# Optimization experiments

Measured on AMD Instinct MI355X. Metric: run time of the kernel, lower is better.

Reference implementation:

```python
import jax, jax.numpy as jnp
import numpy as np

EMBED_DIM = 1024
NUM_HEADS = 16
HEAD_DIM = EMBED_DIM // NUM_HEADS


def setup_inputs() -> dict:
    key = jax.random.key(0)
    ks = jax.random.split(key, 12)
    B, Nq, Nkv, D = 4, 1024, 1024, EMBED_DIM
    s = 1.0 / np.sqrt(D)
    return {
        "query": jax.random.normal(ks[0], (B, Nq, D), jnp.float32),
        "key_value": jax.random.normal(ks[1], (B, Nkv, D), jnp.float32),
        "Wq": jax.random.normal(ks[2], (D, D), jnp.float32) * s,
        "bq": jnp.zeros((D,), jnp.float32),
        "Wk": jax.random.normal(ks[3], (D, D), jnp.float32) * s,
        "bk": jnp.zeros((D,), jnp.float32),
        "Wv": jax.random.normal(ks[4], (D, D), jnp.float32) * s,
        "bv": jnp.zeros((D,), jnp.float32),
        "Wo": jax.random.normal(ks[5], (D, D), jnp.float32) * s,
        "bo": jnp.zeros((D,), jnp.float32),
        "gamma": jnp.ones((D,), jnp.float32),
        "beta": jnp.zeros((D,), jnp.float32),
    }


def reference(query, key_value, Wq, bq, Wk, bk, Wv, bv, Wo, bo, gamma, beta):
    B, Nq, D = query.shape
    Nkv = key_value.shape[1]
    H, Hd = NUM_HEADS, HEAD_DIM
    # projections -> [B, H, N, Hd]
    q = (query @ Wq + bq).reshape(B, Nq, H, Hd).transpose(0, 2, 1, 3)
    k = (key_value @ Wk + bk).reshape(B, Nkv, H, Hd).transpose(0, 2, 1, 3)
    v = (key_value @ Wv + bv).reshape(B, Nkv, H, Hd).transpose(0, 2, 1, 3)
    scores = jnp.einsum("bhqd,bhkd->bhqk", q, k) / jnp.sqrt(jnp.float32(Hd))
    attn = jax.nn.softmax(scores, axis=-1)  # dropout = identity at eval
    out = jnp.einsum("bhqk,bhkd->bhqd", attn, v)
    out = out.transpose(0, 2, 1, 3).reshape(B, Nq, D)
    out = out @ Wo + bo
    # residual + LayerNorm (eps = 1e-5, torch default)
    x = query + out
    mu = jnp.mean(x, axis=-1, keepdims=True)
    var = jnp.mean(jnp.square(x - mu), axis=-1, keepdims=True)
    return (x - mu) / jnp.sqrt(var + 1e-5) * gamma + beta
```

## Files before the change

### kernel.cpp

```cpp
#include <hip/hip_runtime.h>

typedef unsigned short u16;
typedef unsigned int u32;
typedef __attribute__((ext_vector_type(2))) unsigned int u32x2;
typedef __attribute__((ext_vector_type(4))) unsigned short u16x4;
typedef __attribute__((ext_vector_type(8))) short short8;
typedef __attribute__((ext_vector_type(4))) float f32x4;

#define MFMA16(a, b, c) __builtin_amdgcn_mfma_f32_16x16x32_bf16(a, b, c, 0, 0, 0)

__device__ __forceinline__ u16 f2bf(float f) {
  unsigned u = __builtin_bit_cast(unsigned, f);
  u += 0x7fffu + ((u >> 16) & 1u);
  return (u16)(u >> 16);
}

__device__ __forceinline__ float bf2f(u16 b) {
  return __builtin_bit_cast(float, ((u32)b) << 16);
}

__device__ __forceinline__ u32 cvtpk(float lo, float hi) {
  u32 r;
  asm("v_cvt_pk_bf16_f32 %0, %1, %2" : "=v"(r) : "v"(lo), "v"(hi));
  return r;
}

__device__ __forceinline__ float ex2(float x) {
  float r;
  asm("v_exp_f32 %0, %1" : "=v"(r) : "v"(x));
  return r;
}

__device__ __forceinline__ void gl_lds16(const void* g, void* l) {
  __builtin_amdgcn_global_load_lds((const __attribute__((address_space(1))) char*)g,
                                   (__attribute__((address_space(3))) char*)l, 16, 0, 0);
}

__global__ __launch_bounds__(256) void cvt2_k(const float* __restrict__ a,
                                              const float* __restrict__ b,
                                              u16* __restrict__ oa, u16* __restrict__ ob) {
  const int bid = blockIdx.x;
  const float* in = (bid < 4096) ? a : b;
  u16* out = (bid < 4096) ? oa : ob;
  int i = (bid & 4095) * 256 + threadIdx.x;
  float4 v = ((const float4*)in)[i];
  u16x4 o;
  o.x = f2bf(v.x); o.y = f2bf(v.y); o.z = f2bf(v.z); o.w = f2bf(v.w);
  ((u16x4*)out)[i] = o;
}

__global__ __launch_bounds__(256) void wt_k(const float* __restrict__ W0, const float* __restrict__ W1,
                                            const float* __restrict__ W2, const float* __restrict__ W3,
                                            u16* __restrict__ T0, u16* __restrict__ T1,
                                            u16* __restrict__ T2, u16* __restrict__ T3) {
  const float* W; u16* T;
  switch (blockIdx.z) {
    case 0: W = W0; T = T0; break;
    case 1: W = W1; T = T1; break;
    case 2: W = W2; T = T2; break;
    default: W = W3; T = T3; break;
  }
  __shared__ __align__(16) u16 t[64][72];
  const int k0 = blockIdx.y * 64, n0 = blockIdx.x * 64;
  const int tid = threadIdx.x;
  const int r = tid >> 4, c4 = (tid & 15) * 4;
#pragma unroll
  for (int i = 0; i < 4; i++) {
    float4 v = *(const float4*)(W + (k0 + r + i * 16) * 1024 + n0 + c4);
    u16x4 o;
    o.x = f2bf(v.x); o.y = f2bf(v.y); o.z = f2bf(v.z); o.w = f2bf(v.w);
    *(u16x4*)&t[r + i * 16][c4] = o;
  }
  __syncthreads();
#pragma unroll
  for (int i = 0; i < 4; i++) {
    int nr = r + i * 16;
    u16x4 o;
    o.x = t[c4 + 0][nr]; o.y = t[c4 + 1][nr]; o.z = t[c4 + 2][nr]; o.w = t[c4 + 3][nr];
    *(u16x4*)(T + (n0 + nr) * 1024 + k0 + c4) = o;
  }
}

__global__ __launch_bounds__(256, 3) void gemmqkv_k(
    const u16* __restrict__ qbf, const u16* __restrict__ kvbf,
    const u16* __restrict__ Wqt, const u16* __restrict__ Wkt, const u16* __restrict__ Wvt,
    const float* __restrict__ pbq, const float* __restrict__ pbk, const float* __restrict__ pbv,
    u16* __restrict__ Qh, u16* __restrict__ Kh, u16* __restrict__ Vth) {
  const int lin = blockIdx.x;
  const int swz = (lin & 7) * 96 + (lin >> 3);
  const int x = swz & 7, y = (swz >> 3) & 31, z = swz >> 8;

  const u16* A  = (z == 0) ? qbf : kvbf;
  const u16* Bt = (z == 0) ? Wqt : (z == 1 ? Wkt : Wvt);
  const float* bias = (z == 0) ? pbq : (z == 1 ? pbk : pbv);

  __shared__ __align__(16) u16 As[128 * 64];
  __shared__ __align__(16) u16 Bs[128 * 64];
  const int tid = threadIdx.x;
  const int l = tid & 63, w = tid >> 6;
  const int lr = l >> 4, lc = l & 15;
  const int wr = w >> 1, wc = w & 1;
  const int m0 = y * 128, n0 = x * 128;

  f32x4 acc[4][4] = {};

  const int sr = tid >> 2, sc = (tid & 3) * 8;
  const u16* Ag = A + (m0 + sr) * 1024 + sc;
  const u16* Bg = Bt + (n0 + sr) * 1024 + sc;

  for (int k0 = 0; k0 < 1024; k0 += 64) {
    __syncthreads();
    gl_lds16(Ag + k0, As + tid * 8);
    gl_lds16(Ag + 64 * 1024 + k0, As + 2048 + tid * 8);
    gl_lds16(Bg + k0, Bs + tid * 8);
    gl_lds16(Bg + 64 * 1024 + k0, Bs + 2048 + tid * 8);
    gl_lds16(Ag + k0 + 32, As + 4096 + tid * 8);
    gl_lds16(Ag + 64 * 1024 + k0 + 32, As + 6144 + tid * 8);
    gl_lds16(Bg + k0 + 32, Bs + 4096 + tid * 8);
    gl_lds16(Bg + 64 * 1024 + k0 + 32, Bs + 6144 + tid * 8);
    __syncthreads();
    const u16* PA = (z == 2) ? Bs : As;
    const u16* PB = (z == 2) ? As : Bs;
    short8 af[4][2], bf[4][2];
    const int ks8 = lr * 8;
#pragma unroll
    for (int m = 0; m < 4; m++)
#pragma unroll
      for (int h = 0; h < 2; h++)
        af[m][h] = *(const short8*)(PA + h * 4096 + (wr * 64 + m * 16 + lc) * 32 + ks8);
#pragma unroll
    for (int n = 0; n < 4; n++)
#pragma unroll
      for (int h = 0; h < 2; h++)
        bf[n][h] = *(const short8*)(PB + h * 4096 + (wc * 64 + n * 16 + lc) * 32 + ks8);
#pragma unroll
    for (int m = 0; m < 4; m++)
#pragma unroll
      for (int n = 0; n < 4; n++) {
        acc[m][n] = MFMA16(af[m][0], bf[n][0], acc[m][n]);
        acc[m][n] = MFMA16(af[m][1], bf[n][1], acc[m][n]);
      }
  }

  if (z == 2) {
#pragma unroll
    for (int m = 0; m < 4; m++) {
#pragma unroll
      for (int r = 0; r < 4; r++) {
        int ncol = n0 + wr * 64 + m * 16 + lr * 4 + r;
        float bb = bias[ncol];
        int h = ncol >> 6, d = ncol & 63;
#pragma unroll
        for (int n = 0; n < 4; n++) {
          int tok = m0 + wc * 64 + n * 16 + lc;
          Vth[(((tok >> 10) * 16 + h) * 64 + d) * 1024 + (tok & 1023)] =
              f2bf(acc[m][n][r] + bb);
        }
      }
    }
  } else {
    u16* outb = (z == 0) ? Qh : Kh;
    const float scale = (z == 0) ? 0.18033688f : 1.0f;
#pragma unroll
    for (int m = 0; m < 4; m++)
#pragma unroll
      for (int n = 0; n < 4; n++) {
        int ncol = n0 + wc * 64 + n * 16 + lc;
        float bb = bias[ncol];
        int h = ncol >> 6, d = ncol & 63;
#pragma unroll
        for (int r = 0; r < 4; r++) {
          int tok = m0 + wr * 64 + m * 16 + lr * 4 + r;
          outb[(((tok >> 10) * 16 + h) * 1024 + (tok & 1023)) * 64 + d] =
              f2bf((acc[m][n][r] + bb) * scale);
        }
      }
  }
}

__global__ __launch_bounds__(256, 4) void gemmo_k(const u16* __restrict__ A,
                                                  const u16* __restrict__ Bt,
                                                  const float* __restrict__ bias,
                                                  u16* __restrict__ outb) {
  const int lin = blockIdx.x;
  const int swz = (lin & 7) * 64 + (lin >> 3);
  const int x = swz & 15, y = swz >> 4;

  __shared__ __align__(16) u16 As[128 * 64];
  __shared__ __align__(16) u16 Bs[64 * 64];
  const int tid = threadIdx.x;
  const int l = tid & 63, w = tid >> 6;
  const int lr = l >> 4, lc = l & 15;
  const int wr = w >> 1, wc = w & 1;
  const int m0 = y * 128, n0 = x * 64;

  f32x4 acc[4][2] = {};
  const int sc = (tid & 3) * 8;
  const u16* Ag = A + (m0 + (tid >> 2)) * 1024 + sc;
  const u16* Bg = Bt + (n0 + (tid >> 2)) * 1024 + sc;

  for (int k0 = 0; k0 < 1024; k0 += 64) {
    __syncthreads();
    gl_lds16(Ag + k0, As + tid * 8);
    gl_lds16(Ag + 64 * 1024 + k0, As + 2048 + tid * 8);
    gl_lds16(Bg + k0, Bs + tid * 8);
    gl_lds16(Ag + k0 + 32, As + 4096 + tid * 8);
    gl_lds16(Ag + 64 * 1024 + k0 + 32, As + 6144 + tid * 8);
    gl_lds16(Bg + k0 + 32, Bs + 2048 + tid * 8);
    __syncthreads();
    short8 af[4][2], bf[2][2];
    const int ks8 = lr * 8;
#pragma unroll
    for (int m = 0; m < 4; m++)
#pragma unroll
      for (int h = 0; h < 2; h++)
        af[m][h] = *(const short8*)(As + h * 4096 + (wr * 64 + m * 16 + lc) * 32 + ks8);
#pragma unroll
    for (int n = 0; n < 2; n++)
#pragma unroll
      for (int h = 0; h < 2; h++)
        bf[n][h] = *(const short8*)(Bs + h * 2048 + (wc * 32 + n * 16 + lc) * 32 + ks8);
#pragma unroll
    for (int m = 0; m < 4; m++)
#pragma unroll
      for (int n = 0; n < 2; n++) {
        acc[m][n] = MFMA16(af[m][0], bf[n][0], acc[m][n]);
        acc[m][n] = MFMA16(af[m][1], bf[n][1], acc[m][n]);
      }
  }
#pragma unroll
  for (int m = 0; m < 4; m++)
#pragma unroll
    for (int n = 0; n < 2; n++) {
      int ncol = n0 + wc * 32 + n * 16 + lc;
      float bb = bias[ncol];
#pragma unroll
      for (int r = 0; r < 4; r++) {
        int tok = m0 + wr * 64 + m * 16 + lr * 4 + r;
        outb[tok * 1024 + ncol] = f2bf(acc[m][n][r] + bb);
      }
    }
}

__global__ __launch_bounds__(256, 2) void attn_k(const u16* __restrict__ Q,
                                                 const u16* __restrict__ K,
                                                 const u16* __restrict__ Vt,
                                                 u16* __restrict__ O) {
  const int bid = blockIdx.x;
  const int xcd = bid & 7, j = bid >> 3;
  const int bh = xcd + 8 * (j & 7);
  const int q0 = (j >> 3) * 128;
  const int tid = threadIdx.x;
  const int w = tid >> 6, l = tid & 63;
  const int lr = l >> 4, lc = l & 15;
  const u16* Qh = Q + bh * (1024 * 64);
  const u16* Kh = K + bh * (1024 * 64);
  const u16* Vh = Vt + bh * (64 * 1024);

  __shared__ __align__(16) u16 Ks[2][64 * 64];
  __shared__ __align__(16) u16 Vs[2][64 * 64];
  __shared__ __align__(16) u32 Plds[4][2][16][32];

  const int st_row = tid >> 3;
  const int st_cb = (tid & 7) * 16;
  const int sw1 = (st_cb ^ ((st_row & 7) << 4)) >> 1;
  const int st_row2 = st_row + 32;
  const int sw2 = (st_cb ^ ((st_row2 & 7) << 4)) >> 1;

  short8 bq[2][2];
#pragma unroll
  for (int g = 0; g < 2; g++)
#pragma unroll
    for (int ks = 0; ks < 2; ks++)
      bq[g][ks] = *(const short8*)(Qh + (q0 + w * 32 + g * 16 + lc) * 64 + ks * 32 + lr * 8);

  f32x4 oacc[2][4] = {};
  float mrun[2] = {-1e30f, -1e30f};
  float lrun[2] = {0.f, 0.f};

  gl_lds16(Kh + st_row * 64 + sw1, &Ks[0][tid * 8]);
  gl_lds16(Kh + st_row2 * 64 + sw2, &Ks[0][2048 + tid * 8]);
  gl_lds16(Vh + st_row * 1024 + sw1, &Vs[0][tid * 8]);
  gl_lds16(Vh + st_row2 * 1024 + sw2, &Vs[0][2048 + tid * 8]);

  const int xw = (lc & 7) << 2;

  for (int t = 0; t < 16; ++t) {
    const int pb = t & 1;
    if (t < 15) {
      const int kvn = (t + 1) * 64;
      gl_lds16(Kh + (kvn + st_row) * 64 + sw1, &Ks[pb ^ 1][tid * 8]);
      gl_lds16(Kh + (kvn + st_row2) * 64 + sw2, &Ks[pb ^ 1][2048 + tid * 8]);
      gl_lds16(Vh + st_row * 1024 + kvn + sw1, &Vs[pb ^ 1][tid * 8]);
      gl_lds16(Vh + st_row2 * 1024 + kvn + sw2, &Vs[pb ^ 1][2048 + tid * 8]);
      asm volatile("s_waitcnt vmcnt(4)" ::: "memory");
    } else {
      asm volatile("s_waitcnt vmcnt(0)" ::: "memory");
    }
    __builtin_amdgcn_s_barrier();
    asm volatile("" ::: "memory");

    const u16* Kb = Ks[pb];
    const u16* Vb = Vs[pb];

    f32x4 s0[4] = {}, s1[4] = {};
    __builtin_amdgcn_s_setprio(1);
#pragma unroll
    for (int mk = 0; mk < 4; mk++) {
      const int krow = mk * 16 + lc;
      const u16* kp = Kb + krow * 64;
#pragma unroll
      for (int ks = 0; ks < 2; ks++) {
        const int cb = (ks * 64 + lr * 16) ^ ((krow & 7) << 4);
        short8 ak = *(const short8*)(kp + (cb >> 1));
        s0[mk] = MFMA16(ak, bq[0][ks], s0[mk]);
        s1[mk] = MFMA16(ak, bq[1][ks], s1[mk]);
      }
    }
    __builtin_amdgcn_s_setprio(0);

    float mx0, mx1;
    {
      float a = fmaxf(fmaxf(s0[0][0], s0[0][1]), fmaxf(s0[0][2], s0[0][3]));
      float b = fmaxf(fmaxf(s0[1][0], s0[1][1]), fmaxf(s0[1][2], s0[1][3]));
      float c = fmaxf(fmaxf(s0[2][0], s0[2][1]), fmaxf(s0[2][2], s0[2][3]));
      float d = fmaxf(fmaxf(s0[3][0], s0[3][1]), fmaxf(s0[3][2], s0[3][3]));
      mx0 = fmaxf(fmaxf(a, b), fmaxf(c, d));
      float e = fmaxf(fmaxf(s1[0][0], s1[0][1]), fmaxf(s1[0][2], s1[0][3]));
      float f = fmaxf(fmaxf(s1[1][0], s1[1][1]), fmaxf(s1[1][2], s1[1][3]));
      float g2 = fmaxf(fmaxf(s1[2][0], s1[2][1]), fmaxf(s1[2][2], s1[2][3]));
      float h = fmaxf(fmaxf(s1[3][0], s1[3][1]), fmaxf(s1[3][2], s1[3][3]));
      mx1 = fmaxf(fmaxf(e, f), fmaxf(g2, h));
    }

    if (!__all(mx0 <= mrun[0] + 8.f && mx1 <= mrun[1] + 8.f)) {
      mx0 = fmaxf(mx0, __shfl_xor(mx0, 16));
      mx0 = fmaxf(mx0, __shfl_xor(mx0, 32));
      mx1 = fmaxf(mx1, __shfl_xor(mx1, 16));
      mx1 = fmaxf(mx1, __shfl_xor(mx1, 32));
      float mn0 = fmaxf(mrun[0], mx0), mn1 = fmaxf(mrun[1], mx1);
      float al0 = ex2(mrun[0] - mn0), al1 = ex2(mrun[1] - mn1);
      mrun[0] = mn0; mrun[1] = mn1;
      lrun[0] *= al0; lrun[1] *= al1;
      float a0[4], a1[4];
#pragma unroll
      for (int r = 0; r < 4; r++) {
        a0[r] = __shfl(al0, lr * 4 + r);
        a1[r] = __shfl(al1, lr * 4 + r);
      }
#pragma unroll
      for (int nd = 0; nd < 4; nd++)
#pragma unroll
        for (int r = 0; r < 4; r++) {
          oacc[0][nd][r] *= a0[r];
          oacc[1][nd][r] *= a1[r];
        }
    }

#pragma unroll
    for (int mk = 0; mk < 4; mk++)
#pragma unroll
      for (int r = 0; r < 4; r++) {
        s0[mk][r] = ex2(s0[mk][r] - mrun[0]);
        s1[mk][r] = ex2(s1[mk][r] - mrun[1]);
      }
    {
      float a = (s0[0][0] + s0[0][1]) + (s0[0][2] + s0[0][3]);
      float b = (s0[1][0] + s0[1][1]) + (s0[1][2] + s0[1][3]);
      float c = (s0[2][0] + s0[2][1]) + (s0[2][2] + s0[2][3]);
      float d = (s0[3][0] + s0[3][1]) + (s0[3][2] + s0[3][3]);
      lrun[0] += (a + b) + (c + d);
      float e = (s1[0][0] + s1[0][1]) + (s1[0][2] + s1[0][3]);
      float f = (s1[1][0] + s1[1][1]) + (s1[1][2] + s1[1][3]);
      float g2 = (s1[2][0] + s1[2][1]) + (s1[2][2] + s1[2][3]);
      float h = (s1[3][0] + s1[3][1]) + (s1[3][2] + s1[3][3]);
      lrun[1] += (e + f) + (g2 + h);
    }

    u32* PW0 = &Plds[w][0][lc][0];
    u32* PW1 = &Plds[w][1][lc][0];
#pragma unroll
    for (int mk = 0; mk < 4; mk++) {
      const int idx = (mk * 8 + lr * 2) ^ xw;
      u32x2 p0 = {cvtpk(s0[mk][0], s0[mk][1]), cvtpk(s0[mk][2], s0[mk][3])};
      u32x2 p1 = {cvtpk(s1[mk][0], s1[mk][1]), cvtpk(s1[mk][2], s1[mk][3])};
      *(u32x2*)&PW0[idx] = p0;
      *(u32x2*)&PW1[idx] = p1;
    }

    __builtin_amdgcn_s_setprio(1);
#pragma unroll
    for (int ks = 0; ks < 2; ks++) {
      short8 ap0 = *(const short8*)&Plds[w][0][lc][(ks * 16 + lr * 4) ^ xw];
      short8 ap1 = *(const short8*)&Plds[w][1][lc][(ks * 16 + lr * 4) ^ xw];
#pragma unroll
      for (int nd = 0; nd < 4; nd++) {
        const int vrow = nd * 16 + lc;
        const int cb = (ks * 64 + lr * 16) ^ ((vrow & 7) << 4);
        short8 bv = *(const short8*)(Vb + vrow * 64 + (cb >> 1));
        oacc[0][nd] = MFMA16(ap0, bv, oacc[0][nd]);
        oacc[1][nd] = MFMA16(ap1, bv, oacc[1][nd]);
      }
    }
    __builtin_amdgcn_s_setprio(0);

    asm volatile("" ::: "memory");
    __builtin_amdgcn_s_barrier();
  }

  const int b = bh >> 4, h = bh & 15;
#pragma unroll
  for (int g = 0; g < 2; g++) {
    float lsum = lrun[g];
    lsum += __shfl_xor(lsum, 16);
    lsum += __shfl_xor(lsum, 32);
    float inv = 1.f / lsum;
    float invr[4];
#pragma unroll
    for (int r = 0; r < 4; r++) invr[r] = __shfl(inv, lr * 4 + r);
#pragma unroll
    for (int r = 0; r < 4; r++) {
      int row = b * 1024 + q0 + w * 32 + g * 16 + lr * 4 + r;
#pragma unroll
      for (int nd = 0; nd < 4; nd++)
        O[row * 1024 + h * 64 + nd * 16 + lc] = f2bf(oacc[g][nd][r] * invr[r]);
    }
  }
}

__global__ __launch_bounds__(256) void ln_k(const float* __restrict__ q,
                                            const u16* __restrict__ p2,
                                            const float* __restrict__ gamma,
                                            const float* __restrict__ beta,
                                            float* __restrict__ out) {
  const int row = blockIdx.x, tid = threadIdx.x;
  float4 xq = ((const float4*)(q + row * 1024))[tid];
  u16x4 xpb = ((const u16x4*)(p2 + row * 1024))[tid];
  float4 x = {xq.x + bf2f(xpb.x), xq.y + bf2f(xpb.y),
              xq.z + bf2f(xpb.z), xq.w + bf2f(xpb.w)};
  float s = x.x + x.y + x.z + x.w;
#pragma unroll
  for (int off = 1; off < 64; off <<= 1) s += __shfl_xor(s, off);
  __shared__ float red[8];
  const int w = tid >> 6;
  if ((tid & 63) == 0) red[w] = s;
  __syncthreads();
  float mu = (red[0] + red[1] + red[2] + red[3]) * (1.0f / 1024.0f);
  float4 dx = {x.x - mu, x.y - mu, x.z - mu, x.w - mu};
  float s2 = dx.x * dx.x + dx.y * dx.y + dx.z * dx.z + dx.w * dx.w;
#pragma unroll
  for (int off = 1; off < 64; off <<= 1) s2 += __shfl_xor(s2, off);
  if ((tid & 63) == 0) red[4 + w] = s2;
  __syncthreads();
  float var = (red[4] + red[5] + red[6] + red[7]) * (1.0f / 1024.0f);
  float rs = rsqrtf(var + 1e-5f);
  float4 g = ((const float4*)gamma)[tid];
  float4 bb = ((const float4*)beta)[tid];
  float4 o = {dx.x * rs * g.x + bb.x, dx.y * rs * g.y + bb.y,
              dx.z * rs * g.z + bb.z, dx.w * rs * g.w + bb.w};
  ((float4*)(out + row * 1024))[tid] = o;
}

extern "C" void kernel_launch(void* const* d_in, const int* in_sizes, int n_in,
                              void* d_out, int out_size, void* d_ws, size_t ws_size,
                              hipStream_t stream) {
  const float* query = (const float*)d_in[0];
  const float* kv    = (const float*)d_in[1];
  const float* Wq = (const float*)d_in[2];
  const float* bq = (const float*)d_in[3];
  const float* Wk = (const float*)d_in[4];
  const float* bk = (const float*)d_in[5];
  const float* Wv = (const float*)d_in[6];
  const float* bv = (const float*)d_in[7];
  const float* Wo = (const float*)d_in[8];
  const float* bo = (const float*)d_in[9];
  const float* gamma = (const float*)d_in[10];
  const float* beta  = (const float*)d_in[11];
  float* out = (float*)d_out;

  char* ws = (char*)d_ws;
  const size_t MB = 1u << 20;
  u16* qbf  = (u16*)(ws + 0 * MB);
  u16* kvbf = (u16*)(ws + 8 * MB);
  u16* Wqt  = (u16*)(ws + 16 * MB);
  u16* Wkt  = (u16*)(ws + 18 * MB);
  u16* Wvt  = (u16*)(ws + 20 * MB);
  u16* Wot  = (u16*)(ws + 22 * MB);
  u16* Qh   = (u16*)(ws + 24 * MB);
  u16* Kh   = (u16*)(ws + 32 * MB);
  u16* Vth  = (u16*)(ws + 40 * MB);
  u16* attO = (u16*)(ws + 48 * MB);
  u16* p2b  = (u16*)(ws + 56 * MB);

  cvt2_k<<<dim3(8192), dim3(256), 0, stream>>>(query, kv, qbf, kvbf);
  wt_k<<<dim3(16, 16, 4), dim3(256), 0, stream>>>(Wq, Wk, Wv, Wo, Wqt, Wkt, Wvt, Wot);

  gemmqkv_k<<<dim3(768), dim3(256), 0, stream>>>(qbf, kvbf, Wqt, Wkt, Wvt,
                                                 bq, bk, bv, Qh, Kh, Vth);

  attn_k<<<dim3(512), dim3(256), 0, stream>>>(Qh, Kh, Vth, attO);

  gemmo_k<<<dim3(512), dim3(256), 0, stream>>>(attO, Wot, bo, p2b);

  ln_k<<<dim3(4096), dim3(256), 0, stream>>>(query, p2b, gamma, beta, out);
}
```

Before: 101.5 us.

## Double-buffer LDS tiles in QKV and output projection GEMMs with prefetch

Both projection GEMMs now prefetch the next K-tile into a second LDS buffer while computing on the current one. They use explicit vmcnt waits and raw barriers instead of the two syncthreads per iteration. The QKV GEMM's K-step shrinks to 32 so the double buffer keeps the same LDS footprint. The output GEMM doubles its LDS and drops its occupancy target from 4 to 2 blocks, and both kernels raise wave priority around the MFMA block. The goal is to hide global-to-LDS latency, at the cost of more barriers per K and possibly lower occupancy.

```diff
diff --git a/kernel.cpp b/kernel.cpp
--- a/kernel.cpp
+++ b/kernel.cpp
@@ -94,8 +94,8 @@
   const u16* Bt = (z == 0) ? Wqt : (z == 1 ? Wkt : Wvt);
   const float* bias = (z == 0) ? pbq : (z == 1 ? pbk : pbv);
 
-  __shared__ __align__(16) u16 As[128 * 64];
-  __shared__ __align__(16) u16 Bs[128 * 64];
+  __shared__ __align__(16) u16 As[2 * 128 * 32];
+  __shared__ __align__(16) u16 Bs[2 * 128 * 32];
   const int tid = threadIdx.x;
   const int l = tid & 63, w = tid >> 6;
   const int lr = l >> 4, lc = l & 15;
@@ -108,38 +108,48 @@
   const u16* Ag = A + (m0 + sr) * 1024 + sc;
   const u16* Bg = Bt + (n0 + sr) * 1024 + sc;
 
-  for (int k0 = 0; k0 < 1024; k0 += 64) {
-    __syncthreads();
-    gl_lds16(Ag + k0, As + tid * 8);
-    gl_lds16(Ag + 64 * 1024 + k0, As + 2048 + tid * 8);
-    gl_lds16(Bg + k0, Bs + tid * 8);
-    gl_lds16(Bg + 64 * 1024 + k0, Bs + 2048 + tid * 8);
-    gl_lds16(Ag + k0 + 32, As + 4096 + tid * 8);
-    gl_lds16(Ag + 64 * 1024 + k0 + 32, As + 6144 + tid * 8);
-    gl_lds16(Bg + k0 + 32, Bs + 4096 + tid * 8);
-    gl_lds16(Bg + 64 * 1024 + k0 + 32, Bs + 6144 + tid * 8);
-    __syncthreads();
-    const u16* PA = (z == 2) ? Bs : As;
-    const u16* PB = (z == 2) ? As : Bs;
-    short8 af[4][2], bf[4][2];
+  gl_lds16(Ag, As + tid * 8);
+  gl_lds16(Ag + 64 * 1024, As + 2048 + tid * 8);
+  gl_lds16(Bg, Bs + tid * 8);
+  gl_lds16(Bg + 64 * 1024, Bs + 2048 + tid * 8);
+
+  for (int t = 0; t < 32; ++t) {
+    const int pb = t & 1;
+    if (t < 31) {
+      const int kn = (t + 1) * 32;
+      u16* AsN = As + (pb ^ 1) * 4096;
+      u16* BsN = Bs + (pb ^ 1) * 4096;
+      gl_lds16(Ag + kn, AsN + tid * 8);
+      gl_lds16(Ag + 64 * 1024 + kn, AsN + 2048 + tid * 8);
+      gl_lds16(Bg + kn, BsN + tid * 8);
+      gl_lds16(Bg + 64 * 1024 + kn, BsN + 2048 + tid * 8);
+      asm volatile("s_waitcnt vmcnt(4)" ::: "memory");
+    } else {
+      asm volatile("s_waitcnt vmcnt(0)" ::: "memory");
+    }
+    __builtin_amdgcn_s_barrier();
+    asm volatile("" ::: "memory");
+
+    const u16* PA = ((z == 2) ? Bs : As) + pb * 4096;
+    const u16* PB = ((z == 2) ? As : Bs) + pb * 4096;
+    short8 af[4], bf[4];
     const int ks8 = lr * 8;
 #pragma unroll
     for (int m = 0; m < 4; m++)
-#pragma unroll
-      for (int h = 0; h < 2; h++)
-        af[m][h] = *(const short8*)(PA + h * 4096 + (wr * 64 + m * 16 + lc) * 32 + ks8);
+      af[m] = *(const short8*)(PA + (wr * 64 + m * 16 + lc) * 32 + ks8);
 #pragma unroll
     for (int n = 0; n < 4; n++)
-#pragma unroll
-      for (int h = 0; h < 2; h++)
-        bf[n][h] = *(const short8*)(PB + h * 4096 + (wc * 64 + n * 16 + lc) * 32 + ks8);
+      bf[n] = *(const short8*)(PB + (wc * 64 + n * 16 + lc) * 32 + ks8);
+    __builtin_amdgcn_s_setprio(1);
 #pragma unroll
     for (int m = 0; m < 4; m++)
 #pragma unroll
-      for (int n = 0; n < 4; n++) {
-        acc[m][n] = MFMA16(af[m][0], bf[n][0], acc[m][n]);
-        acc[m][n] = MFMA16(af[m][1], bf[n][1], acc[m][n]);
-      }
+      for (int n = 0; n < 4; n++)
+        acc[m][n] = MFMA16(af[m], bf[n], acc[m][n]);
+    __builtin_amdgcn_s_setprio(0);
+
+    asm volatile("" ::: "memory");
+    __builtin_amdgcn_s_barrier();
   }
 
   if (z == 2) {
@@ -178,7 +188,7 @@
   }
 }
 
-__global__ __launch_bounds__(256, 4) void gemmo_k(const u16* __restrict__ A,
+__global__ __launch_bounds__(256, 2) void gemmo_k(const u16* __restrict__ A,
                                                   const u16* __restrict__ Bt,
                                                   const float* __restrict__ bias,
                                                   u16* __restrict__ outb) {
@@ -186,8 +196,8 @@
   const int swz = (lin & 7) * 64 + (lin >> 3);
   const int x = swz & 15, y = swz >> 4;
 
-  __shared__ __align__(16) u16 As[128 * 64];
-  __shared__ __align__(16) u16 Bs[64 * 64];
+  __shared__ __align__(16) u16 As[2 * 128 * 64];
+  __shared__ __align__(16) u16 Bs[2 * 64 * 64];
   const int tid = threadIdx.x;
   const int l = tid & 63, w = tid >> 6;
   const int lr = l >> 4, lc = l & 15;
@@ -199,27 +209,47 @@
   const u16* Ag = A + (m0 + (tid >> 2)) * 1024 + sc;
   const u16* Bg = Bt + (n0 + (tid >> 2)) * 1024 + sc;
 
-  for (int k0 = 0; k0 < 1024; k0 += 64) {
-    __syncthreads();
-    gl_lds16(Ag + k0, As + tid * 8);
-    gl_lds16(Ag + 64 * 1024 + k0, As + 2048 + tid * 8);
-    gl_lds16(Bg + k0, Bs + tid * 8);
-    gl_lds16(Ag + k0 + 32, As + 4096 + tid * 8);
-    gl_lds16(Ag + 64 * 1024 + k0 + 32, As + 6144 + tid * 8);
-    gl_lds16(Bg + k0 + 32, Bs + 2048 + tid * 8);
-    __syncthreads();
+  gl_lds16(Ag, As + tid * 8);
+  gl_lds16(Ag + 64 * 1024, As + 2048 + tid * 8);
+  gl_lds16(Ag + 32, As + 4096 + tid * 8);
+  gl_lds16(Ag + 64 * 1024 + 32, As + 6144 + tid * 8);
+  gl_lds16(Bg, Bs + tid * 8);
+  gl_lds16(Bg + 32, Bs + 2048 + tid * 8);
+
+  for (int t = 0; t < 16; ++t) {
+    const int pb = t & 1;
+    if (t < 15) {
+      const int kn = (t + 1) * 64;
+      u16* AsN = As + (pb ^ 1) * 8192;
+      u16* BsN = Bs + (pb ^ 1) * 4096;
+      gl_lds16(Ag + kn, AsN + tid * 8);
+      gl_lds16(Ag + 64 * 1024 + kn, AsN + 2048 + tid * 8);
+      gl_lds16(Ag + kn + 32, AsN + 4096 + tid * 8);
+      gl_lds16(Ag + 64 * 1024 + kn + 32, AsN + 6144 + tid * 8);
+      gl_lds16(Bg + kn, BsN + tid * 8);
+      gl_lds16(Bg + kn + 32, BsN + 2048 + tid * 8);
+      asm volatile("s_waitcnt vmcnt(6)" ::: "memory");
+    } else {
+      asm volatile("s_waitcnt vmcnt(0)" ::: "memory");
+    }
+    __builtin_amdgcn_s_barrier();
+    asm volatile("" ::: "memory");
+
+    const u16* PA = As + pb * 8192;
+    const u16* PB = Bs + pb * 4096;
     short8 af[4][2], bf[2][2];
     const int ks8 = lr * 8;
 #pragma unroll
     for (int m = 0; m < 4; m++)
 #pragma unroll
       for (int h = 0; h < 2; h++)
-        af[m][h] = *(const short8*)(As + h * 4096 + (wr * 64 + m * 16 + lc) * 32 + ks8);
+        af[m][h] = *(const short8*)(PA + h * 4096 + (wr * 64 + m * 16 + lc) * 32 + ks8);
 #pragma unroll
     for (int n = 0; n < 2; n++)
 #pragma unroll
       for (int h = 0; h < 2; h++)
-        bf[n][h] = *(const short8*)(Bs + h * 2048 + (wc * 32 + n * 16 + lc) * 32 + ks8);
+        bf[n][h] = *(const short8*)(PB + h * 2048 + (wc * 32 + n * 16 + lc) * 32 + ks8);
+    __builtin_amdgcn_s_setprio(1);
 #pragma unroll
     for (int m = 0; m < 4; m++)
 #pragma unroll
@@ -227,6 +257,10 @@
         acc[m][n] = MFMA16(af[m][0], bf[n][0], acc[m][n]);
         acc[m][n] = MFMA16(af[m][1], bf[n][1], acc[m][n]);
       }
+    __builtin_amdgcn_s_setprio(0);
+
+    asm volatile("" ::: "memory");
+    __builtin_amdgcn_s_barrier();
   }
 #pragma unroll
   for (int m = 0; m < 4; m++)
```

Measured after the change: 103.7 us. 2.2% more time.
